# Kernel tuning notes

Hardware: AMD Instinct MI355X
Metric: run time of the kernel (lower is better)

## Reference

```python
import jax, jax.numpy as jnp
import numpy as np

N_NODES = 100000
N_EDGES = 1600000
IN_DIM = 128
HID_DIM = 128


def setup_inputs() -> dict:
    key = jax.random.key(0)
    k_x, k_e, k_w1, k_w2, k_b1, k_b2 = jax.random.split(key, 6)
    x = jax.random.normal(k_x, (N_NODES, IN_DIM), dtype=jnp.float32)
    edge_index = jax.random.randint(k_e, (2, N_EDGES), 0, N_NODES, dtype=jnp.int64)
    # GCNConv params: linear weight (no bias in lin), plus post-aggregation bias
    s1 = 1.0 / np.sqrt(IN_DIM)
    s2 = 1.0 / np.sqrt(HID_DIM)
    W1 = jax.random.uniform(k_w1, (IN_DIM, HID_DIM), jnp.float32, -s1, s1)
    b1 = jnp.zeros((HID_DIM,), jnp.float32)
    W2 = jax.random.uniform(k_w2, (HID_DIM, HID_DIM), jnp.float32, -s2, s2)
    b2 = jnp.zeros((HID_DIM,), jnp.float32)
    return {"x": x, "edge_index": edge_index, "W1": W1, "b1": b1, "W2": W2, "b2": b2}


def _gcn_conv(x, row, col, norm, W, b, n_nodes):
    # h = x W ; out[col] += norm * h[row] ; + b   (PyG GCNConv math)
    h = x @ W
    msg = h[row] * norm[:, None]          # [E+N, H] edge-gathered messages
    out = jax.ops.segment_sum(msg, col, num_segments=n_nodes)
    return out + b


def reference(x, edge_index, W1, b1, W2, b2):
    n = x.shape[0]
    # add self-loops (PyG gcn_norm default: add_self_loops=True, edge_weight=1)
    loop = jnp.arange(n, dtype=edge_index.dtype)
    row = jnp.concatenate([edge_index[0], loop])
    col = jnp.concatenate([edge_index[1], loop])
    # symmetric normalization: deg computed at col (target)
    deg = jax.ops.segment_sum(jnp.ones(row.shape[0], x.dtype), col, num_segments=n)
    dis = jnp.where(deg > 0, jax.lax.rsqrt(jnp.maximum(deg, 1e-30)), 0.0)
    norm = dis[row] * dis[col]            # [E+N]
    h = _gcn_conv(x, row, col, norm, W1, b1, n)
    h = jax.nn.relu(h)
    out = _gcn_conv(h, row, col, norm, W2, b2, n)
    return out
```

## Files before the change

kernel.cpp:

```cpp
#include <hip/hip_runtime.h>

#define NN 100000
#define NE 1600000
#define FD 128
#define NBUK 196
#define EPB 2048
#define NB_E 782
#define NGROUP 6250
#define NCHK 16

typedef unsigned int  u32;
typedef unsigned short u16;
typedef __bf16 bf16x8 __attribute__((ext_vector_type(8)));
typedef float  f32x4v __attribute__((ext_vector_type(4)));

__device__ __forceinline__ u16 f2bf(float f) {
    u32 u = __float_as_uint(f);
    u32 r = (u + 0x7FFFu + ((u >> 16) & 1u)) >> 16;
    return (u16)r;
}

__device__ __forceinline__ void acc2(float& x, float& y, float wt, u32 w) {
    x += wt * __uint_as_float(w << 16);
    y += wt * __uint_as_float(w & 0xffff0000u);
}
__device__ __forceinline__ void acc8(float4& L, float4& H, float wt, uint4 u) {
    acc2(L.x, L.y, wt, u.x); acc2(L.z, L.w, wt, u.y);
    acc2(H.x, H.y, wt, u.z); acc2(H.z, H.w, wt, u.w);
}


__global__ void k_zero(int* __restrict__ p, int n) {
    int i = blockIdx.x * 256 + threadIdx.x;
    if (i < n) p[i] = 0;
}

__global__ __launch_bounds__(256) void k_bhist(const int* __restrict__ col,
                                               int* __restrict__ bcnt) {
    __shared__ int hist[NBUK];
    const int tid = threadIdx.x;
    for (int i = tid; i < NBUK; i += 256) hist[i] = 0;
    __syncthreads();
    const int e0 = blockIdx.x * EPB;
    const int e1 = min(e0 + EPB, NE);
    for (int e = e0 + tid; e < e1; e += 256)
        atomicAdd(&hist[col[e] >> 9], 1);
    __syncthreads();
    for (int i = tid; i < NBUK; i += 256) {
        int h = hist[i];
        if (h) atomicAdd(&bcnt[i], h);
    }
}

__global__ void k_bscan(const int* __restrict__ bcnt, int* __restrict__ bbase,
                        int* __restrict__ bcur, int* __restrict__ row_ptr) {
    if (threadIdx.x == 0 && blockIdx.x == 0) {
        int acc = 0;
        for (int i = 0; i < NBUK; ++i) { int t = bcnt[i]; bbase[i] = acc; bcur[i] = acc; acc += t; }
        bbase[NBUK] = acc;
        row_ptr[NN] = acc;
    }
}

__global__ __launch_bounds__(256) void k_bin(const int* __restrict__ row,
                                             const int* __restrict__ col,
                                             int* __restrict__ bcur,
                                             u32* __restrict__ ebuf) {
    __shared__ int hist[NBUK];
    const int tid = threadIdx.x;
    for (int i = tid; i < NBUK; i += 256) hist[i] = 0;
    __syncthreads();
    const int e0 = blockIdx.x * EPB;
    const int e1 = min(e0 + EPB, NE);
    for (int e = e0 + tid; e < e1; e += 256)
        atomicAdd(&hist[col[e] >> 9], 1);
    __syncthreads();
    for (int i = tid; i < NBUK; i += 256) {
        int c = hist[i];
        hist[i] = c ? atomicAdd(&bcur[i], c) : 0;
    }
    __syncthreads();
    for (int e = e0 + tid; e < e1; e += 256) {
        int c = col[e];
        int pos = atomicAdd(&hist[c >> 9], 1);
        ebuf[pos] = ((u32)row[e] << 9) | (u32)(c & 511);
    }
}

__global__ __launch_bounds__(256) void k_bucket(const u32* __restrict__ ebuf,
                                                const int* __restrict__ bbase,
                                                int* __restrict__ row_ptr,
                                                float* __restrict__ dis,
                                                int* __restrict__ srcs) {
    __shared__ int cnt[512 * NCHK];
    __shared__ int s[256];
    const int tid = threadIdx.x;
    const int b = blockIdx.x;
    const int base = bbase[b], end = bbase[b + 1];

    for (int i = tid; i < 512 * NCHK; i += 256) cnt[i] = 0;
    __syncthreads();
    for (int i = base + tid; i < end; i += 256) {
        u32 p = ebuf[i];
        atomicAdd(&cnt[(p & 511) * NCHK + ((p >> 9) >> 13)], 1);
    }
    __syncthreads();

    int t0 = 0, t1 = 0;
#pragma unroll
    for (int c = 0; c < NCHK; ++c) {
        t0 += cnt[(tid * 2) * NCHK + c];
        t1 += cnt[(tid * 2 + 1) * NCHK + c];
    }
    s[tid] = t0 + t1;
    __syncthreads();
    for (int off = 1; off < 256; off <<= 1) {
        int t = 0;
        if (tid >= off) t = s[tid - off];
        __syncthreads();
        if (tid >= off) s[tid] += t;
        __syncthreads();
    }
    const int excl = (tid == 0) ? 0 : s[tid - 1];

    int cur0 = excl, cur1 = excl + t0;
#pragma unroll
    for (int c = 0; c < NCHK; ++c) {
        int i0 = (tid * 2) * NCHK + c;
        int v = cnt[i0]; cnt[i0] = cur0; cur0 += v;
        int i1 = (tid * 2 + 1) * NCHK + c;
        int w = cnt[i1]; cnt[i1] = cur1; cur1 += w;
    }

    const int v0 = b * 512 + tid * 2;
    if (v0 < NN) {
        row_ptr[v0] = base + excl;
        dis[v0] = rsqrtf((float)t0 + 1.0f);
    }
    if (v0 + 1 < NN) {
        row_ptr[v0 + 1] = base + excl + t0;
        dis[v0 + 1] = rsqrtf((float)t1 + 1.0f);
    }
    __syncthreads();

    for (int i = base + tid; i < end; i += 256) {
        u32 p = ebuf[i];
        int pos = atomicAdd(&cnt[(p & 511) * NCHK + ((p >> 9) >> 13)], 1);
        srcs[base + pos] = (int)(p >> 9);
    }
}

__global__ void k_packW2(const float* __restrict__ W1, const float* __restrict__ W2,
                         u16* __restrict__ Wf1, u16* __restrict__ Wf2) {
    int tid = blockIdx.x * 256 + threadIdx.x;
    if (tid >= 2048) return;
    int l = tid & 63;
    int tq = tid >> 6;
    int q = tq & 3, t = tq >> 2;
    int n = t * 16 + (l & 15);
    int k0 = q * 32 + (l >> 4) * 8;
    u32 p[4], r[4];
    for (int jj = 0; jj < 4; ++jj) {
        u16 lo1 = f2bf(W1[(size_t)(k0 + 2 * jj) * FD + n]);
        u16 hi1 = f2bf(W1[(size_t)(k0 + 2 * jj + 1) * FD + n]);
        p[jj] = (u32)lo1 | ((u32)hi1 << 16);
        u16 lo2 = f2bf(W2[(size_t)(k0 + 2 * jj) * FD + n]);
        u16 hi2 = f2bf(W2[(size_t)(k0 + 2 * jj + 1) * FD + n]);
        r[jj] = (u32)lo2 | ((u32)hi2 << 16);
    }
    *(uint4*)&Wf1[(size_t)tid * 8] = make_uint4(p[0], p[1], p[2], p[3]);
    *(uint4*)&Wf2[(size_t)tid * 8] = make_uint4(r[0], r[1], r[2], r[3]);
}

template <bool F32IN>
__global__ __launch_bounds__(256, 4) void k_gemm_mfma(const void* __restrict__ inv,
                                                      const u16* __restrict__ Wf,
                                                      u16* __restrict__ out) {
    __shared__ u16 Wl[16384];
    const int tid = threadIdx.x;
    {
        const uint4* s = (const uint4*)Wf;
        uint4* d = (uint4*)Wl;
#pragma unroll
        for (int i = 0; i < 8; ++i) d[tid + 256 * i] = s[tid + 256 * i];
    }
    __syncthreads();

    const int wave = tid >> 6, lane = tid & 63;
    const int gid = blockIdx.x * 4 + wave;
    if (gid >= NGROUP) return;
    const int row0 = gid * 16;
    const int lr = lane & 15;
    const int lh = lane >> 4;

    f32x4v acc[8];
#pragma unroll
    for (int t = 0; t < 8; ++t) { f32x4v z = {0.f, 0.f, 0.f, 0.f}; acc[t] = z; }

#pragma unroll
    for (int q = 0; q < 4; ++q) {
        bf16x8 a;
        if (F32IN) {
            const float* arow = (const float*)inv + (size_t)(row0 + lr) * FD + lh * 8 + q * 32;
            float4 f0 = *(const float4*)(arow);
            float4 f1 = *(const float4*)(arow + 4);
            union { bf16x8 v; u16 s[8]; } ua;
            ua.s[0] = f2bf(f0.x); ua.s[1] = f2bf(f0.y);
            ua.s[2] = f2bf(f0.z); ua.s[3] = f2bf(f0.w);
            ua.s[4] = f2bf(f1.x); ua.s[5] = f2bf(f1.y);
            ua.s[6] = f2bf(f1.z); ua.s[7] = f2bf(f1.w);
            a = ua.v;
        } else {
            const u16* arow = (const u16*)inv + (size_t)(row0 + lr) * FD + lh * 8 + q * 32;
            a = *(const bf16x8*)arow;
        }
#pragma unroll
        for (int t = 0; t < 8; ++t) {
            bf16x8 bfr = *(const bf16x8*)(&Wl[(size_t)(t * 4 + q) * 512 + lane * 8]);
            acc[t] = __builtin_amdgcn_mfma_f32_16x16x32_bf16(a, bfr, acc[t], 0, 0, 0);
        }
    }
#pragma unroll
    for (int t = 0; t < 8; ++t) {
#pragma unroll
        for (int j = 0; j < 4; ++j) {
            const int r = row0 + lh * 4 + j;
            out[(size_t)r * FD + t * 16 + lr] = f2bf(acc[t][j]);
        }
    }
}

template <bool BF16OUT>
__global__ __launch_bounds__(256) void k_agg_gather(const u16* __restrict__ hb,
                                                    const float* __restrict__ b,
                                                    const float* __restrict__ dis,
                                                    const int* __restrict__ row_ptr,
                                                    const int* __restrict__ srcs,
                                                    void* __restrict__ outv) {
    const int v = (blockIdx.x * 256 + threadIdx.x) >> 4;
    if (v >= NN) return;
    const int f8 = threadIdx.x & 15;
    const uint4* h4 = (const uint4*)hb;

    const float dv = dis[v];
    float4 aL = ((const float4*)b)[f8 * 2];
    float4 aH = ((const float4*)b)[f8 * 2 + 1];
    {
        const float sl = dv * dv;
        uint4 u = h4[(size_t)v * 16 + f8];
        acc8(aL, aH, sl, u);
    }

    int e = row_ptr[v];
    const int end = row_ptr[v + 1];
    for (; e + 3 < end; e += 4) {
        const int s0 = srcs[e], s1 = srcs[e + 1], s2 = srcs[e + 2], s3 = srcs[e + 3];
        const float w0 = dv * dis[s0];
        const float w1 = dv * dis[s1];
        const float w2 = dv * dis[s2];
        const float w3 = dv * dis[s3];
        const uint4 u0 = h4[(size_t)s0 * 16 + f8];
        const uint4 u1 = h4[(size_t)s1 * 16 + f8];
        const uint4 u2 = h4[(size_t)s2 * 16 + f8];
        const uint4 u3 = h4[(size_t)s3 * 16 + f8];
        acc8(aL, aH, w0, u0); acc8(aL, aH, w1, u1);
        acc8(aL, aH, w2, u2); acc8(aL, aH, w3, u3);
    }
    for (; e < end; ++e) {
        const int s0 = srcs[e];
        const float w0 = dv * dis[s0];
        const uint4 u0 = h4[(size_t)s0 * 16 + f8];
        acc8(aL, aH, w0, u0);
    }

    if (BF16OUT) {
        uint4 p;
        p.x = (u32)f2bf(fmaxf(aL.x, 0.f)) | ((u32)f2bf(fmaxf(aL.y, 0.f)) << 16);
        p.y = (u32)f2bf(fmaxf(aL.z, 0.f)) | ((u32)f2bf(fmaxf(aL.w, 0.f)) << 16);
        p.z = (u32)f2bf(fmaxf(aH.x, 0.f)) | ((u32)f2bf(fmaxf(aH.y, 0.f)) << 16);
        p.w = (u32)f2bf(fmaxf(aH.z, 0.f)) | ((u32)f2bf(fmaxf(aH.w, 0.f)) << 16);
        ((uint4*)outv)[(size_t)v * 16 + f8] = p;
    } else {
        float4* o = (float4*)outv;
        o[(size_t)v * 32 + f8 * 2] = aL;
        o[(size_t)v * 32 + f8 * 2 + 1] = aH;
    }
}


extern "C" void kernel_launch(void* const* d_in, const int* in_sizes, int n_in,
                              void* d_out, int out_size, void* d_ws, size_t ws_size,
                              hipStream_t stream) {
    const float* x  = (const float*)d_in[0];
    const int*   ei = (const int*)d_in[1];
    const float* W1 = (const float*)d_in[2];
    const float* b1 = (const float*)d_in[3];
    const float* W2 = (const float*)d_in[4];
    const float* b2 = (const float*)d_in[5];
    float* out = (float*)d_out;

    const int* row = ei;
    const int* col = ei + NE;

    char* base = (char*)d_ws;
    size_t o = 0;
    auto take = [&](size_t bytes) -> void* {
        void* p = base + o;
        o += (bytes + 255) & ~(size_t)255;
        return p;
    };
    int*   row_ptr = (int*)take((size_t)(NN + 32) * 4);
    int*   bbase   = (int*)take(256 * 4);
    int*   bcur    = (int*)take(256 * 4);
    int*   bcnt    = (int*)take(256 * 4);
    float* dis     = (float*)take((size_t)NN * 4);
    u16*   Wf1     = (u16*)take(16384 * 2);
    u16*   Wf2     = (u16*)take(16384 * 2);
    u16*   hb      = (u16*)take((size_t)NN * FD * 2);
    u16*   aggb    = (u16*)take((size_t)NN * FD * 2);
    int*   srcs    = (int*)take((size_t)NE * 4);
    u32*   ebuf    = (u32*)take((size_t)NE * 4);

    k_zero<<<1, 256, 0, stream>>>(bcnt, 256);
    k_bhist<<<NB_E, 256, 0, stream>>>(col, bcnt);
    k_bscan<<<1, 64, 0, stream>>>(bcnt, bbase, bcur, row_ptr);
    k_bin<<<NB_E, 256, 0, stream>>>(row, col, bcur, ebuf);
    k_bucket<<<NBUK, 256, 0, stream>>>(ebuf, bbase, row_ptr, dis, srcs);

    k_packW2<<<8, 256, 0, stream>>>(W1, W2, Wf1, Wf2);

    k_gemm_mfma<true><<<(NGROUP + 3) / 4, 256, 0, stream>>>(x, Wf1, hb);
    k_agg_gather<true><<<NN * 16 / 256, 256, 0, stream>>>(hb, b1, dis, row_ptr, srcs, aggb);
    k_gemm_mfma<false><<<(NGROUP + 3) / 4, 256, 0, stream>>>(aggb, Wf2, hb);
    k_agg_gather<false><<<NN * 16 / 256, 256, 0, stream>>>(hb, b2, dis, row_ptr, srcs, out);
}
```

Measured before the change: 240.7 us.

## Use fixed-capacity edge buckets and precomputed per-edge weights for aggregation

Replaces the global histogram-plus-scan pass with fixed-capacity buckets (BCAP slots per 512-node bucket). CSR offsets become per-node start and degree arrays. The per-bucket sort drops the source-chunk sub-ordering in favour of a single 512-entry counter. A new kernel precomputes (source, dv*dis[s]) pairs so both aggregation passes read one int2 per edge instead of an index plus a random dis lookup. This saves launches and the histogram pass, but it loses source-locality ordering inside each node's edge list. It also assumes no bucket exceeds its fixed capacity.

New measurement: 229.7 us. 1.05x faster.

```diff
diff --git a/kernel.cpp b/kernel.cpp
--- a/kernel.cpp
+++ b/kernel.cpp
@@ -4,10 +4,10 @@
 #define NE 1600000
 #define FD 128
 #define NBUK 196
-#define EPB 2048
-#define NB_E 782
+#define BCAP 9216
+#define EPBB 8192
+#define NBB 196
 #define NGROUP 6250
-#define NCHK 16
 
 typedef unsigned int  u32;
 typedef unsigned short u16;
@@ -30,36 +30,9 @@
 }
 
 
-__global__ void k_zero(int* __restrict__ p, int n) {
-    int i = blockIdx.x * 256 + threadIdx.x;
-    if (i < n) p[i] = 0;
-}
-
-__global__ __launch_bounds__(256) void k_bhist(const int* __restrict__ col,
-                                               int* __restrict__ bcnt) {
-    __shared__ int hist[NBUK];
-    const int tid = threadIdx.x;
-    for (int i = tid; i < NBUK; i += 256) hist[i] = 0;
-    __syncthreads();
-    const int e0 = blockIdx.x * EPB;
-    const int e1 = min(e0 + EPB, NE);
-    for (int e = e0 + tid; e < e1; e += 256)
-        atomicAdd(&hist[col[e] >> 9], 1);
-    __syncthreads();
-    for (int i = tid; i < NBUK; i += 256) {
-        int h = hist[i];
-        if (h) atomicAdd(&bcnt[i], h);
-    }
-}
-
-__global__ void k_bscan(const int* __restrict__ bcnt, int* __restrict__ bbase,
-                        int* __restrict__ bcur, int* __restrict__ row_ptr) {
-    if (threadIdx.x == 0 && blockIdx.x == 0) {
-        int acc = 0;
-        for (int i = 0; i < NBUK; ++i) { int t = bcnt[i]; bbase[i] = acc; bcur[i] = acc; acc += t; }
-        bbase[NBUK] = acc;
-        row_ptr[NN] = acc;
-    }
+__global__ void k_binit(int* __restrict__ bcur) {
+    int i = threadIdx.x;
+    if (i < NBUK) bcur[i] = i * BCAP;
 }
 
 __global__ __launch_bounds__(256) void k_bin(const int* __restrict__ row,
@@ -70,8 +43,8 @@
     const int tid = threadIdx.x;
     for (int i = tid; i < NBUK; i += 256) hist[i] = 0;
     __syncthreads();
-    const int e0 = blockIdx.x * EPB;
-    const int e1 = min(e0 + EPB, NE);
+    const int e0 = blockIdx.x * EPBB;
+    const int e1 = min(e0 + EPBB, NE);
     for (int e = e0 + tid; e < e1; e += 256)
         atomicAdd(&hist[col[e] >> 9], 1);
     __syncthreads();
@@ -88,31 +61,26 @@
 }
 
 __global__ __launch_bounds__(256) void k_bucket(const u32* __restrict__ ebuf,
-                                                const int* __restrict__ bbase,
-                                                int* __restrict__ row_ptr,
+                                                const int* __restrict__ bcur,
+                                                int* __restrict__ nstart,
+                                                int* __restrict__ ndeg,
                                                 float* __restrict__ dis,
                                                 int* __restrict__ srcs) {
-    __shared__ int cnt[512 * NCHK];
+    __shared__ int lcnt[512];
     __shared__ int s[256];
     const int tid = threadIdx.x;
     const int b = blockIdx.x;
-    const int base = bbase[b], end = bbase[b + 1];
-
-    for (int i = tid; i < 512 * NCHK; i += 256) cnt[i] = 0;
-    __syncthreads();
-    for (int i = base + tid; i < end; i += 256) {
-        u32 p = ebuf[i];
-        atomicAdd(&cnt[(p & 511) * NCHK + ((p >> 9) >> 13)], 1);
-    }
-    __syncthreads();
-
-    int t0 = 0, t1 = 0;
-#pragma unroll
-    for (int c = 0; c < NCHK; ++c) {
-        t0 += cnt[(tid * 2) * NCHK + c];
-        t1 += cnt[(tid * 2 + 1) * NCHK + c];
-    }
-    s[tid] = t0 + t1;
+    const int base = b * BCAP;
+    const int end = bcur[b];
+
+    lcnt[tid] = 0; lcnt[tid + 256] = 0;
+    __syncthreads();
+    for (int i = base + tid; i < end; i += 256)
+        atomicAdd(&lcnt[ebuf[i] & 511], 1);
+    __syncthreads();
+
+    const int c0 = lcnt[tid * 2], c1 = lcnt[tid * 2 + 1];
+    s[tid] = c0 + c1;
     __syncthreads();
     for (int off = 1; off < 256; off <<= 1) {
         int t = 0;
@@ -122,31 +90,43 @@
         __syncthreads();
     }
     const int excl = (tid == 0) ? 0 : s[tid - 1];
-
-    int cur0 = excl, cur1 = excl + t0;
-#pragma unroll
-    for (int c = 0; c < NCHK; ++c) {
-        int i0 = (tid * 2) * NCHK + c;
-        int v = cnt[i0]; cnt[i0] = cur0; cur0 += v;
-        int i1 = (tid * 2 + 1) * NCHK + c;
-        int w = cnt[i1]; cnt[i1] = cur1; cur1 += w;
-    }
+    __syncthreads();
+    lcnt[tid * 2] = excl;
+    lcnt[tid * 2 + 1] = excl + c0;
 
     const int v0 = b * 512 + tid * 2;
     if (v0 < NN) {
-        row_ptr[v0] = base + excl;
-        dis[v0] = rsqrtf((float)t0 + 1.0f);
+        nstart[v0] = base + excl;
+        ndeg[v0] = c0;
+        dis[v0] = rsqrtf((float)c0 + 1.0f);
     }
     if (v0 + 1 < NN) {
-        row_ptr[v0 + 1] = base + excl + t0;
-        dis[v0 + 1] = rsqrtf((float)t1 + 1.0f);
+        nstart[v0 + 1] = base + excl + c0;
+        ndeg[v0 + 1] = c1;
+        dis[v0 + 1] = rsqrtf((float)c1 + 1.0f);
     }
     __syncthreads();
 
     for (int i = base + tid; i < end; i += 256) {
         u32 p = ebuf[i];
-        int pos = atomicAdd(&cnt[(p & 511) * NCHK + ((p >> 9) >> 13)], 1);
+        int pos = atomicAdd(&lcnt[p & 511], 1);
         srcs[base + pos] = (int)(p >> 9);
+    }
+}
+
+__global__ __launch_bounds__(256) void k_wts(const int* __restrict__ nstart,
+                                             const int* __restrict__ ndeg,
+                                             const float* __restrict__ dis,
+                                             const int* __restrict__ srcs,
+                                             int2* __restrict__ ew) {
+    const int v = (blockIdx.x * 256 + threadIdx.x) >> 4;
+    if (v >= NN) return;
+    const int l = threadIdx.x & 15;
+    const float dv = dis[v];
+    const int s0 = nstart[v], d = ndeg[v];
+    for (int e = s0 + l; e < s0 + d; e += 16) {
+        int s = srcs[e];
+        ew[e] = make_int2(s, __float_as_int(dv * dis[s]));
     }
 }
 
@@ -234,8 +214,9 @@
 __global__ __launch_bounds__(256) void k_agg_gather(const u16* __restrict__ hb,
                                                     const float* __restrict__ b,
                                                     const float* __restrict__ dis,
-                                                    const int* __restrict__ row_ptr,
-                                                    const int* __restrict__ srcs,
+                                                    const int* __restrict__ nstart,
+                                                    const int* __restrict__ ndeg,
+                                                    const int2* __restrict__ ew,
                                                     void* __restrict__ outv) {
     const int v = (blockIdx.x * 256 + threadIdx.x) >> 4;
     if (v >= NN) return;
@@ -251,26 +232,23 @@
         acc8(aL, aH, sl, u);
     }
 
-    int e = row_ptr[v];
-    const int end = row_ptr[v + 1];
+    int e = nstart[v];
+    const int end = e + ndeg[v];
     for (; e + 3 < end; e += 4) {
-        const int s0 = srcs[e], s1 = srcs[e + 1], s2 = srcs[e + 2], s3 = srcs[e + 3];
-        const float w0 = dv * dis[s0];
-        const float w1 = dv * dis[s1];
-        const float w2 = dv * dis[s2];
-        const float w3 = dv * dis[s3];
-        const uint4 u0 = h4[(size_t)s0 * 16 + f8];
-        const uint4 u1 = h4[(size_t)s1 * 16 + f8];
-        const uint4 u2 = h4[(size_t)s2 * 16 + f8];
-        const uint4 u3 = h4[(size_t)s3 * 16 + f8];
-        acc8(aL, aH, w0, u0); acc8(aL, aH, w1, u1);
-        acc8(aL, aH, w2, u2); acc8(aL, aH, w3, u3);
+        const int2 p0 = ew[e], p1 = ew[e + 1], p2 = ew[e + 2], p3 = ew[e + 3];
+        const uint4 u0 = h4[(size_t)p0.x * 16 + f8];
+        const uint4 u1 = h4[(size_t)p1.x * 16 + f8];
+        const uint4 u2 = h4[(size_t)p2.x * 16 + f8];
+        const uint4 u3 = h4[(size_t)p3.x * 16 + f8];
+        acc8(aL, aH, __int_as_float(p0.y), u0);
+        acc8(aL, aH, __int_as_float(p1.y), u1);
+        acc8(aL, aH, __int_as_float(p2.y), u2);
+        acc8(aL, aH, __int_as_float(p3.y), u3);
     }
     for (; e < end; ++e) {
-        const int s0 = srcs[e];
-        const float w0 = dv * dis[s0];
-        const uint4 u0 = h4[(size_t)s0 * 16 + f8];
-        acc8(aL, aH, w0, u0);
+        const int2 p0 = ew[e];
+        const uint4 u0 = h4[(size_t)p0.x * 16 + f8];
+        acc8(aL, aH, __int_as_float(p0.y), u0);
     }
 
     if (BF16OUT) {
@@ -309,28 +287,27 @@
         o += (bytes + 255) & ~(size_t)255;
         return p;
     };
-    int*   row_ptr = (int*)take((size_t)(NN + 32) * 4);
-    int*   bbase   = (int*)take(256 * 4);
+    int*   nstart  = (int*)take((size_t)NN * 4);
+    int*   ndeg    = (int*)take((size_t)NN * 4);
     int*   bcur    = (int*)take(256 * 4);
-    int*   bcnt    = (int*)take(256 * 4);
     float* dis     = (float*)take((size_t)NN * 4);
     u16*   Wf1     = (u16*)take(16384 * 2);
     u16*   Wf2     = (u16*)take(16384 * 2);
     u16*   hb      = (u16*)take((size_t)NN * FD * 2);
     u16*   aggb    = (u16*)take((size_t)NN * FD * 2);
-    int*   srcs    = (int*)take((size_t)NE * 4);
-    u32*   ebuf    = (u32*)take((size_t)NE * 4);
-
-    k_zero<<<1, 256, 0, stream>>>(bcnt, 256);
-    k_bhist<<<NB_E, 256, 0, stream>>>(col, bcnt);
-    k_bscan<<<1, 64, 0, stream>>>(bcnt, bbase, bcur, row_ptr);
-    k_bin<<<NB_E, 256, 0, stream>>>(row, col, bcur, ebuf);
-    k_bucket<<<NBUK, 256, 0, stream>>>(ebuf, bbase, row_ptr, dis, srcs);
+    int*   srcs    = (int*)take((size_t)NBUK * BCAP * 4);
+    int2*  ew      = (int2*)take((size_t)NBUK * BCAP * 8);
+    u32*   ebuf    = (u32*)take((size_t)NBUK * BCAP * 4);
+
+    k_binit<<<1, 256, 0, stream>>>(bcur);
+    k_bin<<<NBB, 256, 0, stream>>>(row, col, bcur, ebuf);
+    k_bucket<<<NBUK, 256, 0, stream>>>(ebuf, bcur, nstart, ndeg, dis, srcs);
+    k_wts<<<NGROUP, 256, 0, stream>>>(nstart, ndeg, dis, srcs, ew);
 
     k_packW2<<<8, 256, 0, stream>>>(W1, W2, Wf1, Wf2);
 
     k_gemm_mfma<true><<<(NGROUP + 3) / 4, 256, 0, stream>>>(x, Wf1, hb);
-    k_agg_gather<true><<<NN * 16 / 256, 256, 0, stream>>>(hb, b1, dis, row_ptr, srcs, aggb);
+    k_agg_gather<true><<<NN * 16 / 256, 256, 0, stream>>>(hb, b1, dis, nstart, ndeg, ew, aggb);
     k_gemm_mfma<false><<<(NGROUP + 3) / 4, 256, 0, stream>>>(aggb, Wf2, hb);
-    k_agg_gather<false><<<NN * 16 / 256, 256, 0, stream>>>(hb, b2, dis, row_ptr, srcs, out);
-}
+    k_agg_gather<false><<<NN * 16 / 256, 256, 0, stream>>>(hb, b2, dis, nstart, ndeg, ew, out);
+}
```
